# Optimization experiments

Hardware: AMD Instinct MI355X
Metric: run time of the kernel (lower is better)

Reference implementation:

```python
import jax, jax.numpy as jnp
import numpy as np


def _convert(idx, mask, arr, n_layout):
    # atom_layout.convertV2: flatten the first n_layout (layout) axes of arr,
    # gather with idx, zero out entries where mask is False.
    flat = arr.reshape((-1,) + arr.shape[n_layout:])
    out = flat[idx]
    m = mask.reshape(mask.shape + (1,) * (out.ndim - mask.ndim))
    return jnp.where(m, out, 0).astype(out.dtype)


def _ln(x, scale):
    # LayerNorm(bias=False), eps=1e-5
    mu = jnp.mean(x, axis=-1, keepdims=True)
    var = jnp.var(x, axis=-1, keepdims=True)
    return (x - mu) * jax.lax.rsqrt(var + 1e-5) * scale


def setup_inputs() -> dict:
    key = jax.random.key(0)
    ks = jax.random.split(key, 32)
    T, A, S, Q, K = 768, 24, 576, 32, 128  # tokens, atoms/token, subsets, queries, keys
    CA, CP = 128, 16  # per_atom_channels, per_atom_pair_channels
    d = {}
    d['trunk_single_cond'] = jax.random.normal(ks[0], (T, 384), jnp.float32)
    d['trunk_pair_cond'] = jax.random.normal(ks[1], (T, T, 128), jnp.float32)
    d['ref_ops'] = jax.random.normal(ks[2], (T, A, 3), jnp.float32)
    d['ref_mask'] = (jax.random.uniform(ks[3], (T, A)) < 0.9).astype(jnp.float32)
    d['ref_element'] = jax.random.randint(ks[4], (T, A), 0, 128, jnp.int32)
    d['ref_charge'] = jax.random.normal(ks[5], (T, A), jnp.float32)
    d['ref_atom_name_chars'] = jax.random.randint(ks[6], (T, A, 4), 0, 64, jnp.int32)
    d['ref_space_uid'] = jax.random.randint(ks[7], (T, A), 0, T, jnp.int32)
    d['queries_mask'] = jax.random.uniform(ks[8], (S, Q)) < 0.9
    d['acat_atoms_to_q_gather_idxs'] = jax.random.randint(ks[9], (S, Q), 0, T * A, jnp.int32)
    d['acat_atoms_to_q_gather_mask'] = jax.random.uniform(ks[10], (S, Q)) < 0.9
    d['acat_q_to_k_gather_idxs'] = jax.random.randint(ks[11], (S, K), 0, S * Q, jnp.int32)
    d['acat_q_to_k_gather_mask'] = jax.random.uniform(ks[12], (S, K)) < 0.9
    d['acat_t_to_q_gather_idxs'] = jax.random.randint(ks[13], (S, Q), 0, T, jnp.int32)
    d['acat_t_to_q_gather_mask'] = jax.random.uniform(ks[14], (S, Q)) < 0.9
    d['acat_t_to_k_gather_idxs'] = jax.random.randint(ks[15], (S, K), 0, T, jnp.int32)
    d['acat_t_to_k_gather_mask'] = jax.random.uniform(ks[16], (S, K)) < 0.9
    def w(k, i, o):
        return jax.random.normal(k, (i, o), jnp.float32) * (1.0 / np.sqrt(i)).astype(np.float32)
    d['w_pos'] = w(ks[17], 3, CA)
    d['w_maskw'] = w(ks[18], 1, CA)
    d['w_elem'] = w(ks[19], 128, CA)
    d['w_chg'] = w(ks[20], 1, CA)
    d['w_name'] = w(ks[21], 256, CA)
    d['ln_s_scale'] = jnp.ones((384,), jnp.float32)
    d['w_ts'] = w(ks[22], 384, CA)
    d['w_row'] = w(ks[23], CA, CP)
    d['w_col'] = w(ks[24], CA, CP)
    d['ln_p_scale'] = jnp.ones((128,), jnp.float32)
    d['w_tp'] = w(ks[25], 128, CP)
    d['w_off'] = w(ks[26], 3, CP)
    d['w_dist'] = w(ks[27], 1, CP)
    d['w_valid'] = w(ks[28], 1, CP)
    d['w_m1'] = w(ks[29], CP, CP)
    d['w_m2'] = w(ks[30], CP, CP)
    d['w_m3'] = w(ks[31], CP, CP)
    return d


def reference(trunk_single_cond, trunk_pair_cond, ref_ops, ref_mask, ref_element,
              ref_charge, ref_atom_name_chars, ref_space_uid, queries_mask,
              acat_atoms_to_q_gather_idxs, acat_atoms_to_q_gather_mask,
              acat_q_to_k_gather_idxs, acat_q_to_k_gather_mask,
              acat_t_to_q_gather_idxs, acat_t_to_q_gather_mask,
              acat_t_to_k_gather_idxs, acat_t_to_k_gather_mask,
              w_pos, w_maskw, w_elem, w_chg, w_name, ln_s_scale, w_ts,
              w_row, w_col, ln_p_scale, w_tp, w_off, w_dist, w_valid,
              w_m1, w_m2, w_m3):
    # --- per-atom conditioning on token_atoms layout (T, A, CA) ---
    act = ref_ops @ w_pos
    act = act + ref_mask[:, :, None] * w_maskw[0]
    act = act + w_elem[ref_element]                      # one_hot(128) @ W == row gather
    act = act + jnp.arcsinh(ref_charge)[:, :, None] * w_chg[0]
    wn = w_name.reshape(4, 64, -1)                        # 4 name chars x 64-way one-hot
    act = act + wn[jnp.arange(4), ref_atom_name_chars].sum(axis=2)
    token_atoms_single_cond = act * ref_mask[:, :, None]

    # --- single conditioning in queries / keys layouts ---
    queries_single_cond = _convert(acat_atoms_to_q_gather_idxs, acat_atoms_to_q_gather_mask,
                                   token_atoms_single_cond, 2)
    tsc = _ln(trunk_single_cond, ln_s_scale) @ w_ts
    queries_single_cond = queries_single_cond + _convert(acat_t_to_q_gather_idxs,
                                                         acat_t_to_q_gather_mask, tsc, 1)
    keys_single_cond = _convert(acat_q_to_k_gather_idxs, acat_q_to_k_gather_mask,
                                queries_single_cond, 2)
    keys_mask = _convert(acat_q_to_k_gather_idxs, acat_q_to_k_gather_mask, queries_mask, 2)

    # --- pair activations (S, Q, K, CP) ---
    row_act = jax.nn.relu(queries_single_cond) @ w_row
    # pair_cond_keys_input is the same gather as keys_single_cond
    col_act = jax.nn.relu(keys_single_cond) @ w_col
    pair_act = row_act[:, :, None, :] + col_act[:, None, :, :]

    tpc = _ln(trunk_pair_cond, ln_p_scale) @ w_tp        # (T, T, CP)
    T = trunk_pair_cond.shape[0]
    pidx = T * acat_t_to_q_gather_idxs[:, :, None] + acat_t_to_k_gather_idxs[:, None, :]
    pmask = acat_t_to_q_gather_mask[:, :, None] & acat_t_to_k_gather_mask[:, None, :]
    pair_add = _convert(pidx, pmask, tpc, 2)

    q_pos = _convert(acat_atoms_to_q_gather_idxs, acat_atoms_to_q_gather_mask, ref_ops, 2)
    q_uid = _convert(acat_atoms_to_q_gather_idxs, acat_atoms_to_q_gather_mask, ref_space_uid, 2)
    k_pos = _convert(acat_q_to_k_gather_idxs, acat_q_to_k_gather_mask, q_pos, 2)
    # NB: source gathers keys uid from raw ref_space_uid (flattened) with q->k idxs
    k_uid = _convert(acat_q_to_k_gather_idxs, acat_q_to_k_gather_mask, ref_space_uid, 2)

    valid = (q_uid[:, :, None] == k_uid[:, None, :])[:, :, :, None].astype(pair_act.dtype)
    offsets = q_pos[:, :, None, :] - k_pos[:, None, :, :]
    pair_add = pair_add + (offsets @ w_off) * valid
    sq = jnp.sum(offsets * offsets, axis=-1, keepdims=True)
    pair_add = pair_add + ((1.0 / (1.0 + sq)) @ w_dist) * valid
    pair_add = pair_add + valid @ w_valid
    pair_act = pair_act + pair_add

    p2 = jax.nn.relu(pair_act) @ w_m1
    p2 = jax.nn.relu(p2) @ w_m2
    pair_act = pair_act + jax.nn.relu(p2) @ w_m3
    return (queries_single_cond, pair_act, keys_mask, keys_single_cond)
```

## Files before the change

### kernel.cpp

```cpp
#include <hip/hip_runtime.h>

#define T_ 768
#define A_ 24
#define S_ 576
#define Q_ 32
#define K_ 128
#define CA_ 128
#define CP_ 16

typedef const float* fp;

__device__ float g_wv[2048];
__device__ float g_cw[16];

__global__ void k_token_atoms(fp ref_ops, fp ref_mask, const int* ref_element,
                              fp ref_charge, const int* name_chars,
                              fp w_pos, fp w_maskw, fp w_elem, fp w_chg, fp w_name,
                              float* ws_tok)
{
    int ta = blockIdx.x;
    int c  = threadIdx.x;
    float p0 = ref_ops[ta*3+0];
    float p1 = ref_ops[ta*3+1];
    float p2 = ref_ops[ta*3+2];
    float m  = ref_mask[ta];
    int   e  = ref_element[ta];
    float chg= asinhf(ref_charge[ta]);
    float acc = p0*w_pos[0*CA_+c] + p1*w_pos[1*CA_+c] + p2*w_pos[2*CA_+c];
    acc += m * w_maskw[c];
    acc += w_elem[e*CA_+c];
    acc += chg * w_chg[c];
    #pragma unroll
    for (int j=0;j<4;j++){
        int v = name_chars[ta*4+j];
        acc += w_name[(j*64+v)*CA_+c];
    }
    ws_tok[ta*CA_+c] = acc * m;
}

__global__ void k_tsc(fp trunk_single, fp ln_s_scale, fp w_ts, float* ws_tsc)
{
    int t = blockIdx.x; int c = threadIdx.x;
    __shared__ float xh[384];
    __shared__ float red[128];
    float x0 = trunk_single[t*384 + c];
    float x1 = trunk_single[t*384 + 128 + c];
    float x2 = trunk_single[t*384 + 256 + c];
    red[c] = x0+x1+x2; __syncthreads();
    for (int off=64; off>0; off>>=1){ if (c<off) red[c]+=red[c+off]; __syncthreads(); }
    float mu = red[0] / 384.f;
    __syncthreads();
    float d0=x0-mu, d1=x1-mu, d2=x2-mu;
    red[c] = d0*d0+d1*d1+d2*d2; __syncthreads();
    for (int off=64; off>0; off>>=1){ if (c<off) red[c]+=red[c+off]; __syncthreads(); }
    float rs = rsqrtf(red[0]/384.f + 1e-5f);
    __syncthreads();
    xh[c]     = d0*rs*ln_s_scale[c];
    xh[c+128] = d1*rs*ln_s_scale[c+128];
    xh[c+256] = d2*rs*ln_s_scale[c+256];
    __syncthreads();
    float acc=0.f;
    for (int i=0;i<384;i++) acc += xh[i]*w_ts[i*CA_+c];
    ws_tsc[t*CA_+c]=acc;
}

__global__ void k_queries(const float* ws_tok, const float* ws_tsc,
                          const int* a2q_idx, const int* a2q_mask,
                          const int* t2q_idx, const int* t2q_mask,
                          fp w_row,
                          float* ws_q, float* ws_rowa, float* out_q)
{
    int i = blockIdx.x; int c = threadIdx.x;
    __shared__ float r[128];
    __shared__ float part[128];
    float v = 0.f;
    if (a2q_mask[i]) v += ws_tok[a2q_idx[i]*CA_ + c];
    if (t2q_mask[i]) v += ws_tsc[t2q_idx[i]*CA_ + c];
    ws_q[i*CA_+c] = v;
    out_q[i*CA_+c] = v;
    r[c] = fmaxf(v, 0.f);
    __syncthreads();
    int j = c & 15, ch = c >> 4;
    float acc = 0.f;
    #pragma unroll
    for (int ii=0; ii<16; ii++) acc += r[ch*16+ii]*w_row[(ch*16+ii)*16+j];
    part[c] = acc; __syncthreads();
    if (c < 16){
        float a2 = 0.f;
        #pragma unroll
        for (int ch2=0; ch2<8; ch2++) a2 += part[ch2*16+c];
        ws_rowa[i*16+c] = a2;
    }
}

__global__ void k_keys(const float* ws_q, const int* q2k_idx, const int* q2k_mask,
                       const int* queries_mask, fp w_col,
                       float* ws_cola, float* out_keys, float* out_kmask)
{
    int i = blockIdx.x; int c = threadIdx.x;
    __shared__ float r[128];
    __shared__ float part[128];
    int gi = q2k_idx[i]; int m = q2k_mask[i];
    float v = m ? ws_q[gi*CA_+c] : 0.f;
    out_keys[i*CA_+c] = v;
    if (c==0) out_kmask[i] = (m && queries_mask[gi]) ? 1.f : 0.f;
    r[c] = fmaxf(v, 0.f);
    __syncthreads();
    int j = c & 15, ch = c >> 4;
    float acc = 0.f;
    #pragma unroll
    for (int ii=0; ii<16; ii++) acc += r[ch*16+ii]*w_col[(ch*16+ii)*16+j];
    part[c] = acc; __syncthreads();
    if (c < 16){
        float a2 = 0.f;
        #pragma unroll
        for (int ch2=0; ch2<8; ch2++) a2 += part[ch2*16+c];
        ws_cola[i*16+c] = a2;
    }
}

__global__ void k_tpc_prep(fp w_tp, fp ln_p_scale)
{
    int i = threadIdx.x;
    for (int r = i; r < 2048; r += 256) g_wv[r] = w_tp[r] * ln_p_scale[r >> 4];
    __syncthreads();
    if (i < 16){
        float s = 0.f;
        #pragma unroll
        for (int c = 0; c < 128; c++) s += g_wv[c*16 + i];
        g_cw[i] = s;
    }
}

__global__ __launch_bounds__(256) void k_tpc2(fp trunk_pair, float* ws_tpc)
{
    int pid = blockIdx.x*256 + threadIdx.x;
    const float4* row = (const float4*)(trunk_pair + (size_t)pid*128);
    float pj[16];
    #pragma unroll
    for (int j=0;j<16;j++) pj[j]=0.f;
    float s1=0.f, s2=0.f;
    for (int c4=0;c4<32;c4++){
        float4 x = row[c4];
        s1 += (x.x+x.y)+(x.z+x.w);
        s2 += x.x*x.x + x.y*x.y + x.z*x.z + x.w*x.w;
        const float* w0 = g_wv + c4*64;
        #pragma unroll
        for (int j=0;j<16;j++)
            pj[j] += x.x*w0[j] + x.y*w0[16+j] + x.z*w0[32+j] + x.w*w0[48+j];
    }
    float mu  = s1*(1.f/128.f);
    float var = s2*(1.f/128.f) - mu*mu;
    float rs  = rsqrtf(var + 1e-5f);
    float4* dst = (float4*)(ws_tpc + (size_t)pid*16);
    #pragma unroll
    for (int j4=0;j4<4;j4++){
        float4 o;
        o.x = rs*(pj[j4*4+0] - mu*g_cw[j4*4+0]);
        o.y = rs*(pj[j4*4+1] - mu*g_cw[j4*4+1]);
        o.z = rs*(pj[j4*4+2] - mu*g_cw[j4*4+2]);
        o.w = rs*(pj[j4*4+3] - mu*g_cw[j4*4+3]);
        dst[j4]=o;
    }
}

__global__ void k_qgeo(fp ref_ops, const int* ref_uid, const int* a2q_idx, const int* a2q_mask,
                       float* qpos, int* quid)
{
    int i = blockIdx.x*256 + threadIdx.x;
    if (i >= S_*Q_) return;
    int gi = a2q_idx[i]; int m = a2q_mask[i];
    qpos[i*3+0] = m ? ref_ops[gi*3+0] : 0.f;
    qpos[i*3+1] = m ? ref_ops[gi*3+1] : 0.f;
    qpos[i*3+2] = m ? ref_ops[gi*3+2] : 0.f;
    quid[i] = m ? ref_uid[gi] : 0;
}

__global__ void k_kgeo(const float* qpos, const int* ref_uid, const int* q2k_idx, const int* q2k_mask,
                       float* kpos, int* kuid)
{
    int i = blockIdx.x*256 + threadIdx.x;
    if (i >= S_*K_) return;
    int gi = q2k_idx[i]; int m = q2k_mask[i];
    kpos[i*3+0] = m ? qpos[gi*3+0] : 0.f;
    kpos[i*3+1] = m ? qpos[gi*3+1] : 0.f;
    kpos[i*3+2] = m ? qpos[gi*3+2] : 0.f;
    kuid[i] = m ? ref_uid[gi] : 0;
}

__global__ __launch_bounds__(256) void k_pair2(
    const float* ws_rowa, const float* ws_cola, const float* ws_tpc,
    const float* qpos, const float* kpos, const int* quid, const int* kuid,
    const int* t2q_idx, const int* t2q_mask, const int* t2k_idx, const int* t2k_mask,
    fp w_off, fp w_dist, fp w_valid, fp w_m1, fp w_m2, fp w_m3,
    float* out_pair)
{
    int tid = threadIdx.x;
    int sq  = blockIdx.x*4 + (tid>>6);
    int k0  = (tid&63)*2;
    int s   = sq >> 5;
    int sk0 = s*K_ + k0;

    float p0[16], p1[16];
    const float4* ra = (const float4*)(ws_rowa + (size_t)sq*16);
    const float4* ca = (const float4*)(ws_cola + (size_t)sk0*16);
    #pragma unroll
    for (int j4=0;j4<4;j4++){
        float4 a  = ra[j4];
        float4 b0 = ca[j4];
        float4 b1 = ca[4+j4];
        p0[j4*4+0]=a.x+b0.x; p0[j4*4+1]=a.y+b0.y; p0[j4*4+2]=a.z+b0.z; p0[j4*4+3]=a.w+b0.w;
        p1[j4*4+0]=a.x+b1.x; p1[j4*4+1]=a.y+b1.y; p1[j4*4+2]=a.z+b1.z; p1[j4*4+3]=a.w+b1.w;
    }

    int tqm = t2q_mask[sq];
    int tq  = t2q_idx[sq];
    int2 km = *(const int2*)(t2k_mask + sk0);
    int2 kv = *(const int2*)(t2k_idx + sk0);
    if (tqm && km.x){
        const float4* tp = (const float4*)(ws_tpc + (size_t)(tq*T_ + kv.x)*16);
        #pragma unroll
        for (int j4=0;j4<4;j4++){
            float4 v = tp[j4];
            p0[j4*4+0]+=v.x; p0[j4*4+1]+=v.y; p0[j4*4+2]+=v.z; p0[j4*4+3]+=v.w;
        }
    }
    if (tqm && km.y){
        const float4* tp = (const float4*)(ws_tpc + (size_t)(tq*T_ + kv.y)*16);
        #pragma unroll
        for (int j4=0;j4<4;j4++){
            float4 v = tp[j4];
            p1[j4*4+0]+=v.x; p1[j4*4+1]+=v.y; p1[j4*4+2]+=v.z; p1[j4*4+3]+=v.w;
        }
    }

    float qx=qpos[sq*3+0], qy=qpos[sq*3+1], qz=qpos[sq*3+2];
    int   qu=quid[sq];
    const float2* kp = (const float2*)(kpos + (size_t)sk0*3);
    float2 ka=kp[0], kb=kp[1], kc=kp[2];
    int2 ku = *(const int2*)(kuid + sk0);
    {
        float ox=qx-ka.x, oy=qy-ka.y, oz=qz-kb.x;
        float val = (qu==ku.x) ? 1.f : 0.f;
        float invd = val/(1.f + ox*ox+oy*oy+oz*oz);
        ox*=val; oy*=val; oz*=val;
        #pragma unroll
        for (int j=0;j<16;j++)
            p0[j] += ox*w_off[j] + oy*w_off[16+j] + oz*w_off[32+j]
                   + invd*w_dist[j] + val*w_valid[j];
    }
    {
        float ox=qx-kb.y, oy=qy-kc.x, oz=qz-kc.y;
        float val = (qu==ku.y) ? 1.f : 0.f;
        float invd = val/(1.f + ox*ox+oy*oy+oz*oz);
        ox*=val; oy*=val; oz*=val;
        #pragma unroll
        for (int j=0;j<16;j++)
            p1[j] += ox*w_off[j] + oy*w_off[16+j] + oz*w_off[32+j]
                   + invd*w_dist[j] + val*w_valid[j];
    }

    float h0[16], h1[16];
    #pragma unroll
    for (int j=0;j<16;j++){ h0[j]=0.f; h1[j]=0.f; }
    #pragma unroll
    for (int i=0;i<16;i++){
        float r0=fmaxf(p0[i],0.f), r1=fmaxf(p1[i],0.f);
        #pragma unroll
        for (int j=0;j<16;j++){ float w=w_m1[i*16+j]; h0[j]+=r0*w; h1[j]+=r1*w; }
    }
    float g0[16], g1[16];
    #pragma unroll
    for (int j=0;j<16;j++){ g0[j]=0.f; g1[j]=0.f; }
    #pragma unroll
    for (int i=0;i<16;i++){
        float r0=fmaxf(h0[i],0.f), r1=fmaxf(h1[i],0.f);
        #pragma unroll
        for (int j=0;j<16;j++){ float w=w_m2[i*16+j]; g0[j]+=r0*w; g1[j]+=r1*w; }
    }
    #pragma unroll
    for (int i=0;i<16;i++){
        float r0=fmaxf(g0[i],0.f), r1=fmaxf(g1[i],0.f);
        #pragma unroll
        for (int j=0;j<16;j++){ float w=w_m3[i*16+j]; p0[j]+=r0*w; p1[j]+=r1*w; }
    }

    float4* dst = (float4*)(out_pair + ((size_t)sq*K_ + k0)*16);
    #pragma unroll
    for (int j4=0;j4<4;j4++){
        float4 v0; v0.x=p0[j4*4+0]; v0.y=p0[j4*4+1]; v0.z=p0[j4*4+2]; v0.w=p0[j4*4+3];
        float4 v1; v1.x=p1[j4*4+0]; v1.y=p1[j4*4+1]; v1.z=p1[j4*4+2]; v1.w=p1[j4*4+3];
        dst[j4]   = v0;
        dst[4+j4] = v1;
    }
}

extern "C" void kernel_launch(void* const* d_in, const int* in_sizes, int n_in,
                              void* d_out, int out_size, void* d_ws, size_t ws_size,
                              hipStream_t stream)
{
    fp trunk_single = (fp)d_in[0];
    fp trunk_pair   = (fp)d_in[1];
    fp ref_ops      = (fp)d_in[2];
    fp ref_mask     = (fp)d_in[3];
    const int* ref_element  = (const int*)d_in[4];
    fp ref_charge   = (fp)d_in[5];
    const int* name_chars   = (const int*)d_in[6];
    const int* ref_uid      = (const int*)d_in[7];
    const int* queries_mask = (const int*)d_in[8];
    const int* a2q_idx = (const int*)d_in[9];
    const int* a2q_mask= (const int*)d_in[10];
    const int* q2k_idx = (const int*)d_in[11];
    const int* q2k_mask= (const int*)d_in[12];
    const int* t2q_idx = (const int*)d_in[13];
    const int* t2q_mask= (const int*)d_in[14];
    const int* t2k_idx = (const int*)d_in[15];
    const int* t2k_mask= (const int*)d_in[16];
    fp w_pos  = (fp)d_in[17];
    fp w_maskw= (fp)d_in[18];
    fp w_elem = (fp)d_in[19];
    fp w_chg  = (fp)d_in[20];
    fp w_name = (fp)d_in[21];
    fp ln_s   = (fp)d_in[22];
    fp w_ts   = (fp)d_in[23];
    fp w_row  = (fp)d_in[24];
    fp w_col  = (fp)d_in[25];
    fp ln_p   = (fp)d_in[26];
    fp w_tp   = (fp)d_in[27];
    fp w_off  = (fp)d_in[28];
    fp w_dist = (fp)d_in[29];
    fp w_valid= (fp)d_in[30];
    fp w_m1   = (fp)d_in[31];
    fp w_m2   = (fp)d_in[32];
    fp w_m3   = (fp)d_in[33];

    float* out = (float*)d_out;
    float* out_q     = out;
    float* out_pair  = out + 2359296;
    float* out_kmask = out + 2359296 + 37748736;
    float* out_keys  = out + 2359296 + 37748736 + 73728;

    float* ws = (float*)d_ws;
    float* ws_tok = ws;
    float* ws_tsc = ws_tok + 2359296;
    float* ws_q   = ws_tsc + 98304;
    float* ws_rowa= ws_q   + 2359296;
    float* ws_cola= ws_rowa+ 294912;
    float* ws_tpc = ws_cola+ 1179648;
    float* ws_qpos= ws_tpc + 9437184;
    float* ws_kpos= ws_qpos+ 55296;
    int*   ws_quid= (int*)(ws_kpos + 221184);
    int*   ws_kuid= ws_quid + 18432;

    k_token_atoms<<<T_*A_, 128, 0, stream>>>(ref_ops, ref_mask, ref_element, ref_charge,
        name_chars, w_pos, w_maskw, w_elem, w_chg, w_name, ws_tok);
    k_tsc<<<T_, 128, 0, stream>>>(trunk_single, ln_s, w_ts, ws_tsc);
    k_queries<<<S_*Q_, 128, 0, stream>>>(ws_tok, ws_tsc, a2q_idx, a2q_mask, t2q_idx, t2q_mask,
        w_row, ws_q, ws_rowa, out_q);
    k_keys<<<S_*K_, 128, 0, stream>>>(ws_q, q2k_idx, q2k_mask, queries_mask, w_col,
        ws_cola, out_keys, out_kmask);
    k_tpc_prep<<<1, 256, 0, stream>>>(w_tp, ln_p);
    k_tpc2<<<(T_*T_)/256, 256, 0, stream>>>(trunk_pair, ws_tpc);
    k_qgeo<<<(S_*Q_+255)/256, 256, 0, stream>>>(ref_ops, ref_uid, a2q_idx, a2q_mask, ws_qpos, ws_quid);
    k_kgeo<<<(S_*K_+255)/256, 256, 0, stream>>>(ws_qpos, ref_uid, q2k_idx, q2k_mask, ws_kpos, ws_kuid);
    k_pair2<<<(S_*Q_*K_)/512, 256, 0, stream>>>(ws_rowa, ws_cola, ws_tpc, ws_qpos, ws_kpos,
        ws_quid, ws_kuid, t2q_idx, t2q_mask, t2k_idx, t2k_mask,
        w_off, w_dist, w_valid, w_m1, w_m2, w_m3, out_pair);
}
```

Baseline: 876.3 us.

## Stage trunk pair rows through swizzled double-buffered LDS tiles for coalesced loads

The pair-conditioning LayerNorm+projection kernel previously had each thread read its own 512-byte row directly, which gives strided, uncoalesced global access. It now loads each 256-row block cooperatively in four 32-channel chunks into XOR-swizzled shared-memory tiles, so each load instruction reads contiguous memory. The tiles are double-buffered so the next chunk's load is issued before the current chunk is consumed. This costs 64 KB of LDS per block and adds barriers, which may lower occupancy.

```diff
diff --git a/kernel.cpp b/kernel.cpp
--- a/kernel.cpp
+++ b/kernel.cpp
@@ -134,25 +134,53 @@
 
 __global__ __launch_bounds__(256) void k_tpc2(fp trunk_pair, float* ws_tpc)
 {
-    int pid = blockIdx.x*256 + threadIdx.x;
-    const float4* row = (const float4*)(trunk_pair + (size_t)pid*128);
+    __shared__ float4 tile[2][256*8];
+    int t = threadIdx.x;
+    const float4* src = (const float4*)trunk_pair + (size_t)blockIdx.x * (256*32);
+
+    #pragma unroll
+    for (int p=0;p<8;p++){
+        int li = p*256 + t;
+        int r = li>>3, c4 = li&7;
+        tile[0][r*8 + (c4 ^ (r&7))] = src[r*32 + c4];
+    }
+
     float pj[16];
     #pragma unroll
     for (int j=0;j<16;j++) pj[j]=0.f;
     float s1=0.f, s2=0.f;
-    for (int c4=0;c4<32;c4++){
-        float4 x = row[c4];
-        s1 += (x.x+x.y)+(x.z+x.w);
-        s2 += x.x*x.x + x.y*x.y + x.z*x.z + x.w*x.w;
-        const float* w0 = g_wv + c4*64;
-        #pragma unroll
-        for (int j=0;j<16;j++)
-            pj[j] += x.x*w0[j] + x.y*w0[16+j] + x.z*w0[32+j] + x.w*w0[48+j];
-    }
+    int r7 = t & 7;
+
+    #pragma unroll
+    for (int ch=0; ch<4; ch++){
+        __syncthreads();
+        if (ch < 3){
+            int nb = (ch+1)&1;
+            #pragma unroll
+            for (int p=0;p<8;p++){
+                int li = p*256 + t;
+                int r = li>>3, c4 = li&7;
+                tile[nb][r*8 + (c4 ^ (r&7))] = src[r*32 + (ch+1)*8 + c4];
+            }
+        }
+        int cb = ch&1;
+        #pragma unroll
+        for (int c4=0;c4<8;c4++){
+            float4 x = tile[cb][t*8 + (c4 ^ r7)];
+            s1 += (x.x+x.y)+(x.z+x.w);
+            s2 += x.x*x.x + x.y*x.y + x.z*x.z + x.w*x.w;
+            const float* w0 = g_wv + (ch*8+c4)*64;
+            #pragma unroll
+            for (int j=0;j<16;j++)
+                pj[j] += x.x*w0[j] + x.y*w0[16+j] + x.z*w0[32+j] + x.w*w0[48+j];
+        }
+    }
+
     float mu  = s1*(1.f/128.f);
     float var = s2*(1.f/128.f) - mu*mu;
     float rs  = rsqrtf(var + 1e-5f);
-    float4* dst = (float4*)(ws_tpc + (size_t)pid*16);
+    size_t pid = (size_t)blockIdx.x*256 + t;
+    float4* dst = (float4*)(ws_tpc + pid*16);
     #pragma unroll
     for (int j4=0;j4<4;j4++){
         float4 o;
```

New measurement: 1.718 ms. 1.96x slower.

## Stage trunk pair rows in shared memory and keep projection weights in registers

Applied to the files above, without the earlier changes.

Replaces the one-thread-per-row trunk pair LayerNorm+projection kernel with a tiled version. Each block loads 64-row tiles with coalesced float4 loads into padded shared memory, computes the row statistics cooperatively, and has each thread compute one output channel for four rows using a 128-entry weight column held in registers. The old kernel did strided per-thread row reads, with every thread walking the whole weight matrix. The change targets the memory-bound 300MB read. It adds register pressure from the 128-float weight array, plus several barriers per tile.

```diff
diff --git a/kernel.cpp b/kernel.cpp
--- a/kernel.cpp
+++ b/kernel.cpp
@@ -132,35 +132,81 @@
     }
 }
 
-__global__ __launch_bounds__(256) void k_tpc2(fp trunk_pair, float* ws_tpc)
-{
-    int pid = blockIdx.x*256 + threadIdx.x;
-    const float4* row = (const float4*)(trunk_pair + (size_t)pid*128);
-    float pj[16];
-    #pragma unroll
-    for (int j=0;j<16;j++) pj[j]=0.f;
-    float s1=0.f, s2=0.f;
-    for (int c4=0;c4<32;c4++){
-        float4 x = row[c4];
-        s1 += (x.x+x.y)+(x.z+x.w);
-        s2 += x.x*x.x + x.y*x.y + x.z*x.z + x.w*x.w;
-        const float* w0 = g_wv + c4*64;
-        #pragma unroll
-        for (int j=0;j<16;j++)
-            pj[j] += x.x*w0[j] + x.y*w0[16+j] + x.z*w0[32+j] + x.w*w0[48+j];
-    }
-    float mu  = s1*(1.f/128.f);
-    float var = s2*(1.f/128.f) - mu*mu;
-    float rs  = rsqrtf(var + 1e-5f);
-    float4* dst = (float4*)(ws_tpc + (size_t)pid*16);
-    #pragma unroll
-    for (int j4=0;j4<4;j4++){
-        float4 o;
-        o.x = rs*(pj[j4*4+0] - mu*g_cw[j4*4+0]);
-        o.y = rs*(pj[j4*4+1] - mu*g_cw[j4*4+1]);
-        o.z = rs*(pj[j4*4+2] - mu*g_cw[j4*4+2]);
-        o.w = rs*(pj[j4*4+3] - mu*g_cw[j4*4+3]);
-        dst[j4]=o;
+#define TPC_ROWS 64
+#define TPC_PITCH 132
+__global__ __launch_bounds__(256, 2) void k_tpc3(fp trunk_pair, float* ws_tpc)
+{
+    __shared__ float xs[TPC_ROWS * TPC_PITCH];
+    __shared__ float p1s[256], p2s[256];
+    __shared__ float mus[TPC_ROWS], rss[TPC_ROWS];
+
+    int t  = threadIdx.x;
+    int j  = t & 15;
+    int rg = t >> 4;
+
+    float wj[128];
+    #pragma unroll
+    for (int c = 0; c < 128; c++) wj[c] = g_wv[c*16 + j];
+    float cwj = g_cw[j];
+
+    #pragma unroll 1
+    for (int it = 0; it < 4; it++){
+        int tile = blockIdx.x*4 + it;
+        const float4* src = (const float4*)trunk_pair + (size_t)tile * (TPC_ROWS*32);
+
+        __syncthreads();
+        #pragma unroll
+        for (int p = 0; p < 8; p++){
+            int li = p*256 + t;
+            int r = li >> 5, c4 = li & 31;
+            float4 v = src[li];
+            *(float4*)(xs + r*TPC_PITCH + c4*4) = v;
+        }
+        __syncthreads();
+        {
+            int rm = t >> 2, mq = t & 3;
+            const float* xr = xs + rm*TPC_PITCH + mq*32;
+            float s1 = 0.f, s2 = 0.f;
+            #pragma unroll
+            for (int i = 0; i < 8; i++){
+                float4 v = *(const float4*)(xr + i*4);
+                s1 += (v.x+v.y)+(v.z+v.w);
+                s2 += v.x*v.x+v.y*v.y+v.z*v.z+v.w*v.w;
+            }
+            p1s[t] = s1; p2s[t] = s2;
+        }
+        __syncthreads();
+        if (t < TPC_ROWS){
+            float s1 = p1s[t*4]+p1s[t*4+1]+p1s[t*4+2]+p1s[t*4+3];
+            float s2 = p2s[t*4]+p2s[t*4+1]+p2s[t*4+2]+p2s[t*4+3];
+            float mu = s1*(1.f/128.f);
+            float var = s2*(1.f/128.f) - mu*mu;
+            mus[t] = mu; rss[t] = rsqrtf(var + 1e-5f);
+        }
+        __syncthreads();
+        float pj0=0.f, pj1=0.f, pj2=0.f, pj3=0.f;
+        const float* x0 = xs + (rg*4+0)*TPC_PITCH;
+        const float* x1 = xs + (rg*4+1)*TPC_PITCH;
+        const float* x2 = xs + (rg*4+2)*TPC_PITCH;
+        const float* x3 = xs + (rg*4+3)*TPC_PITCH;
+        #pragma unroll
+        for (int c4 = 0; c4 < 32; c4++){
+            float4 a = *(const float4*)(x0 + c4*4);
+            float4 b = *(const float4*)(x1 + c4*4);
+            float4 c = *(const float4*)(x2 + c4*4);
+            float4 d = *(const float4*)(x3 + c4*4);
+            float w0 = wj[c4*4+0], w1 = wj[c4*4+1], w2 = wj[c4*4+2], w3 = wj[c4*4+3];
+            pj0 += a.x*w0 + a.y*w1 + a.z*w2 + a.w*w3;
+            pj1 += b.x*w0 + b.y*w1 + b.z*w2 + b.w*w3;
+            pj2 += c.x*w0 + c.y*w1 + c.z*w2 + c.w*w3;
+            pj3 += d.x*w0 + d.y*w1 + d.z*w2 + d.w*w3;
+        }
+        size_t rowbase = (size_t)tile*TPC_ROWS + rg*4;
+        float* dst = ws_tpc + rowbase*16 + j;
+        dst[0]  = rss[rg*4+0]*(pj0 - mus[rg*4+0]*cwj);
+        dst[16] = rss[rg*4+1]*(pj1 - mus[rg*4+1]*cwj);
+        dst[32] = rss[rg*4+2]*(pj2 - mus[rg*4+2]*cwj);
+        dst[48] = rss[rg*4+3]*(pj3 - mus[rg*4+3]*cwj);
     }
 }
 
@@ -360,7 +406,7 @@
     k_keys<<<S_*K_, 128, 0, stream>>>(ws_q, q2k_idx, q2k_mask, queries_mask, w_col,
         ws_cola, out_keys, out_kmask);
     k_tpc_prep<<<1, 256, 0, stream>>>(w_tp, ln_p);
-    k_tpc2<<<(T_*T_)/256, 256, 0, stream>>>(trunk_pair, ws_tpc);
+    k_tpc3<<<(T_*T_)/(TPC_ROWS*4), 256, 0, stream>>>(trunk_pair, ws_tpc);
     k_qgeo<<<(S_*Q_+255)/256, 256, 0, stream>>>(ref_ops, ref_uid, a2q_idx, a2q_mask, ws_qpos, ws_quid);
     k_kgeo<<<(S_*K_+255)/256, 256, 0, stream>>>(ws_qpos, ref_uid, q2k_idx, q2k_mask, ws_kpos, ws_kuid);
     k_pair2<<<(S_*Q_*K_)/512, 256, 0, stream>>>(ws_rowa, ws_cola, ws_tpc, ws_qpos, ws_kpos,
```

After: 707.5 us. 1.24x faster.
